# Optimization experiments

Measured on AMD Instinct MI355X. Metric: run time of the kernel, lower is better.

## Reference

```python
import jax, jax.numpy as jnp
import numpy as np

D_MODEL = 1024
NUM_HEADS = 16
HEAD_DIM = D_MODEL // NUM_HEADS
B, L = 4, 4096


def _linear(x, w, b):
    # torch nn.Linear: y = x @ w.T + b, w: [out, in]
    return jnp.einsum('bld,od->blo', x, w) + b


def _elu_feature_map(x):
    return jax.nn.elu(x) + 1.0


def setup_inputs() -> dict:
    key = jax.random.key(0)
    ks = jax.random.split(key, 11)
    s = 1.0 / np.sqrt(D_MODEL)
    inp = {
        'query': jax.random.normal(ks[0], (B, L, D_MODEL), jnp.float32),
        'key': jax.random.normal(ks[1], (B, L, D_MODEL), jnp.float32),
        'value': jax.random.normal(ks[2], (B, L, D_MODEL), jnp.float32),
        'wq': jax.random.uniform(ks[3], (D_MODEL, D_MODEL), jnp.float32, -s, s),
        'bq': jax.random.uniform(ks[4], (D_MODEL,), jnp.float32, -s, s),
        'wk': jax.random.uniform(ks[5], (D_MODEL, D_MODEL), jnp.float32, -s, s),
        'bk': jax.random.uniform(ks[6], (D_MODEL,), jnp.float32, -s, s),
        'wv': jax.random.uniform(ks[7], (D_MODEL, D_MODEL), jnp.float32, -s, s),
        'bv': jax.random.uniform(ks[8], (D_MODEL,), jnp.float32, -s, s),
        'wo': jax.random.uniform(ks[9], (D_MODEL, D_MODEL), jnp.float32, -s, s),
        'bo': jax.random.uniform(ks[10], (D_MODEL,), jnp.float32, -s, s),
    }
    return inp


def reference(query, key, value, wq, bq, wk, bk, wv, bv, wo, bo):
    Bsz, Lq, _ = query.shape
    # project and split heads -> [B, H, L, hd]
    def split_heads(x):
        return x.reshape(Bsz, -1, NUM_HEADS, HEAD_DIM).transpose(0, 2, 1, 3)
    Q = split_heads(_linear(query, wq, bq))
    K = split_heads(_linear(key, wk, bk))
    V = split_heads(_linear(value, wv, bv))
    Q = _elu_feature_map(Q)
    K = _elu_feature_map(K)
    # KV: [B, H, hd, hd]
    KV = jnp.einsum('bhld,bhle->bhde', K, V)
    Ksum = K.sum(axis=2)  # [B, H, hd]
    Z = 1.0 / (jnp.einsum('bhld,bhd->bhl', Q, Ksum) + 1e-6)  # [B, H, Lq]
    out = jnp.einsum('bhld,bhde->bhle', Q, KV) * Z[..., None]
    out = out.transpose(0, 2, 1, 3).reshape(Bsz, Lq, D_MODEL)
    return _linear(out, wo, bo)
```

## Files before the change

### kernel.cpp

```cpp
#include <hip/hip_runtime.h>
#include <hip/hip_bf16.h>

typedef _Float16 half8 __attribute__((ext_vector_type(8)));
typedef _Float16 half4 __attribute__((ext_vector_type(4)));
typedef float f32x4 __attribute__((ext_vector_type(4)));

#define KDIM 1024
#define NDIM 1024
#define MROWS 16384

#define GLD_LDS16(g, l)                                                  \
  __builtin_amdgcn_global_load_lds(                                      \
      (const __attribute__((address_space(1))) void*)(g),                \
      (__attribute__((address_space(3))) void*)(l), 16, 0, 0)

__global__ __launch_bounds__(256)
void cvt_f32_to_f16(const float* __restrict__ src, _Float16* __restrict__ dst,
                    int n8) {
  for (int i = blockIdx.x * 256 + threadIdx.x; i < n8; i += gridDim.x * 256) {
    float4 f0 = ((const float4*)src)[2 * i];
    float4 f1 = ((const float4*)src)[2 * i + 1];
    half8 h;
    h[0] = (_Float16)f0.x; h[1] = (_Float16)f0.y;
    h[2] = (_Float16)f0.z; h[3] = (_Float16)f0.w;
    h[4] = (_Float16)f1.x; h[5] = (_Float16)f1.y;
    h[6] = (_Float16)f1.z; h[7] = (_Float16)f1.w;
    ((half8*)dst)[i] = h;
  }
}

__global__ __launch_bounds__(256)
void cvt_w(const float* __restrict__ s0, _Float16* __restrict__ d0,
           const float* __restrict__ s1, _Float16* __restrict__ d1,
           const float* __restrict__ s2, _Float16* __restrict__ d2,
           const float* __restrict__ s3, _Float16* __restrict__ d3) {
  const float* src;
  _Float16* dst;
  switch (blockIdx.y) {
    case 0: src = s0; dst = d0; break;
    case 1: src = s1; dst = d1; break;
    case 2: src = s2; dst = d2; break;
    default: src = s3; dst = d3; break;
  }
  size_t i = (size_t)blockIdx.x * 256 + threadIdx.x;
  float4 f = ((const float4*)src)[i];
  half4 h;
  h[0] = (_Float16)f.x; h[1] = (_Float16)f.y;
  h[2] = (_Float16)f.z; h[3] = (_Float16)f.w;
  ((half4*)dst)[i] = h;
}

template <int ACT, int MODE, typename TOUT>
__global__ __launch_bounds__(512, 2)
void gemm_8ph(const _Float16* __restrict__ X, const _Float16* __restrict__ W,
              const float* __restrict__ bias, TOUT* __restrict__ Y,
              const _Float16* __restrict__ KVTx) {
  __shared__ char smem[131072];
  _Float16* As = (_Float16*)smem;
  _Float16* Bs = (_Float16*)(smem + 65536);

  const int tid  = threadIdx.x;
  const int lane = tid & 63;
  const int w    = tid >> 6;
  const int wm   = w >> 2;
  const int wn   = w & 3;

  const int bid = blockIdx.x;
  const int wid = (bid & 7) * 32 + (bid >> 3);
  const int m0  = (wid >> 2) * 256;
  const int n0  = (wid & 3) * 256;

  const int srow = lane >> 2;
  const int gsl  = (lane & 3) ^ ((lane >> 3) & 3);
  const _Float16* gA = X + (size_t)(m0 + w * 32 + srow) * KDIM + gsl * 8;
  const _Float16* gB = W + (size_t)(n0 + w * 32 + srow) * KDIM + gsl * 8;

#define STG(OPD, GSRC, T, KH, D)                                             \
  {                                                                          \
    _Float16* ldst = OPD + ((D) * 2 + (KH)) * 8192 + (w * 32) * 32;          \
    const _Float16* gs = GSRC + (size_t)(T) * 64 + (KH) * 32;                \
    GLD_LDS16(gs, ldst);                                                     \
    GLD_LDS16(gs + (size_t)16 * KDIM, ldst + 16 * 32);                       \
  }

  const int rsl = ((lane >> 4) ^ ((lane >> 1) & 3)) << 4;

#define RDA(DST, D, KH, MH)                                                  \
  _Pragma("unroll") for (int mi = 0; mi < 4; ++mi) {                         \
    int r = wm * 128 + (MH) * 64 + mi * 16 + (lane & 15);                    \
    DST[mi] = *(const half8*)((const char*)As + ((D) * 2 + (KH)) * 16384 +   \
                              r * 64 + rsl);                                 \
  }
#define RDB(D, KH)                                                           \
  _Pragma("unroll") for (int ni = 0; ni < 4; ++ni) {                         \
    int r = wn * 64 + ni * 16 + (lane & 15);                                 \
    b[ni] = *(const half8*)((const char*)Bs + ((D) * 2 + (KH)) * 16384 +     \
                            r * 64 + rsl);                                   \
  }
#define MM(AV, MH)                                                           \
  __builtin_amdgcn_s_setprio(1);                                             \
  _Pragma("unroll") for (int mi = 0; mi < 4; ++mi)                           \
    _Pragma("unroll") for (int ni = 0; ni < 4; ++ni)                         \
      acc[(MH) * 4 + mi][ni] = __builtin_amdgcn_mfma_f32_16x16x32_f16(       \
          AV[mi], b[ni], acc[(MH) * 4 + mi][ni], 0, 0, 0);                   \
  __builtin_amdgcn_s_setprio(0);

  f32x4 acc[8][4] = {};
  half8 a0[4], a1[4], b[4];

  STG(As, gA, 0, 0, 0); STG(Bs, gB, 0, 0, 0);
  STG(As, gA, 0, 1, 0); STG(Bs, gB, 0, 1, 0);

  for (int T = 0; T < 16; ++T) {
    const int d = T & 1, e = d ^ 1;
    asm volatile("s_waitcnt vmcnt(4)" ::: "memory");
    asm volatile("s_barrier" ::: "memory");
    RDA(a0, d, 0, 0);
    RDB(d, 0);
    if (T < 15) STG(As, gA, T + 1, 0, e);
    MM(a0, 0);
    RDA(a1, d, 0, 1);
    if (T < 15) STG(Bs, gB, T + 1, 0, e);
    MM(a1, 1);
    if (T < 15) { asm volatile("s_waitcnt vmcnt(4)" ::: "memory"); }
    else        { asm volatile("s_waitcnt vmcnt(0)" ::: "memory"); }
    asm volatile("s_barrier" ::: "memory");
    RDA(a0, d, 1, 0);
    RDB(d, 1);
    if (T < 15) STG(As, gA, T + 1, 1, e);
    MM(a0, 0);
    RDA(a1, d, 1, 1);
    if (T < 15) STG(Bs, gB, T + 1, 1, e);
    MM(a1, 1);
  }
#undef STG
#undef RDA
#undef RDB
#undef MM

  if constexpr (MODE == 2) {
    __syncthreads();
    _Float16* Cw = (_Float16*)(smem + w * 16384);
#pragma unroll
    for (int ni = 0; ni < 4; ++ni) {
      int dcol = ni * 16 + (lane & 15);
      float bv = bias[n0 + wn * 64 + dcol];
#pragma unroll
      for (int mi = 0; mi < 8; ++mi) {
#pragma unroll
        for (int i = 0; i < 4; ++i) {
          int rowr = mi * 16 + ((lane >> 4) << 2) + i;
          float v = acc[mi][ni][i] + bv;
          v = (v > 0.f) ? (v + 1.f) : __expf(v);
          int byte = rowr * 128 + dcol * 2;
          byte ^= (rowr & 7) << 4;
          *(_Float16*)((char*)Cw + byte) = (_Float16)v;
        }
      }
    }
    asm volatile("s_waitcnt lgkmcnt(0)" ::: "memory");
    __builtin_amdgcn_sched_barrier(0);
    const int bh0 = ((m0 >> 12) << 4) + (n0 >> 6);
    const _Float16* kvp = KVTx + (size_t)(bh0 + wn) * 5120;
#pragma unroll
    for (int half = 0; half < 2; ++half) {
      f32x4 acc2[4][5] = {};
#pragma unroll
      for (int kk = 0; kk < 2; ++kk) {
        half8 afr2[4], bfr2[5];
#pragma unroll
        for (int m = 0; m < 4; ++m) {
          int rowr = half * 64 + m * 16 + (lane & 15);
          int byte = rowr * 128 + kk * 64 + ((lane >> 4) << 4);
          byte ^= (rowr & 7) << 4;
          afr2[m] = *(const half8*)((const char*)Cw + byte);
        }
#pragma unroll
        for (int n = 0; n < 5; ++n) {
          int row = n * 16 + (lane & 15);
          bfr2[n] = *(const half8*)(kvp + row * 64 + kk * 32 + ((lane >> 4) << 3));
        }
#pragma unroll
        for (int m = 0; m < 4; ++m)
#pragma unroll
          for (int n = 0; n < 5; ++n)
            acc2[m][n] = __builtin_amdgcn_mfma_f32_16x16x32_f16(
                afr2[m], bfr2[n], acc2[m][n], 0, 0, 0);
      }
#pragma unroll
      for (int m = 0; m < 4; ++m) {
#pragma unroll
        for (int i = 0; i < 4; ++i) {
          float dn = __shfl(acc2[m][4][i], lane & 48);
          float z  = 1.f / (dn + 1e-6f);
          size_t row = (size_t)m0 + wm * 128 + half * 64 + m * 16 +
                       ((lane >> 4) << 2) + i;
#pragma unroll
          for (int n = 0; n < 4; ++n) {
            int col = n0 + wn * 64 + n * 16 + (lane & 15);
            Y[row * NDIM + col] = (TOUT)(acc2[m][n][i] * z);
          }
        }
      }
    }
    return;
  }

#pragma unroll
  for (int ni = 0; ni < 4; ++ni) {
    int col  = n0 + wn * 64 + ni * 16 + (lane & 15);
    float bv = bias[col];
#pragma unroll
    for (int mi = 0; mi < 8; ++mi) {
      int r0 = m0 + wm * 128 + mi * 16 + ((lane >> 4) << 2);
      if constexpr (MODE == 1) {
        int bb = r0 >> 12;
        int l0 = r0 & 4095;
        half4 hv;
#pragma unroll
        for (int i = 0; i < 4; ++i) {
          float v = acc[mi][ni][i] + bv;
          if constexpr (ACT == 1) v = (v > 0.f) ? (v + 1.f) : __expf(v);
          hv[i] = (_Float16)v;
        }
        *(half4*)((_Float16*)Y + ((size_t)(bb * 1024 + col)) * 4096 + l0) = hv;
      } else {
#pragma unroll
        for (int i = 0; i < 4; ++i) {
          float v = acc[mi][ni][i] + bv;
          if constexpr (ACT == 1) v = (v > 0.f) ? (v + 1.f) : __expf(v);
          Y[(size_t)(r0 + i) * NDIM + col] = (TOUT)v;
        }
      }
    }
  }
}

__global__ __launch_bounds__(256, 2)
void kv_mfma(const _Float16* __restrict__ KT, const _Float16* __restrict__ VT,
             _Float16* __restrict__ pKV) {
  const int bh = blockIdx.x;
  const int ch = blockIdx.y;
  const int tid  = threadIdx.x;
  const int lane = tid & 63;
  const int w    = tid >> 6;

  __shared__ _Float16 As[64 * 64];
  __shared__ _Float16 Bs[64 * 64];

  const int lr = lane >> 3;
  const int ls = (lane & 7) ^ lr;
  const size_t lbase = (size_t)ch * 1024 + ls * 8;
  const _Float16* gA = VT + (size_t)(bh * 64 + w * 16 + lr) * 4096 + lbase;
  const _Float16* gB = KT + (size_t)(bh * 64 + w * 16 + lr) * 4096 + lbase;
  _Float16* ldsA = As + (w * 16) * 64;
  _Float16* ldsB = Bs + (w * 16) * 64;

  half8 aones;
#pragma unroll
  for (int j = 0; j < 8; ++j) aones[j] = (lane & 15) == 0 ? (_Float16)1.0f : (_Float16)0.0f;

  f32x4 acc[5] = {};

  for (int k0 = 0; k0 < 1024; k0 += 64) {
    __syncthreads();
#pragma unroll
    for (int c = 0; c < 2; ++c) {
      GLD_LDS16(gA + k0 + (size_t)(c * 8) * 4096, ldsA + c * 8 * 64);
      GLD_LDS16(gB + k0 + (size_t)(c * 8) * 4096, ldsB + c * 8 * 64);
    }
    __syncthreads();

    half8 afr[4][2], bfr[2];
#pragma unroll
    for (int m = 0; m < 4; ++m)
#pragma unroll
      for (int kk = 0; kk < 2; ++kk) {
        int row  = m * 16 + (lane & 15);
        int byte = row * 128 + ((lane >> 4) << 4) + kk * 64;
        byte ^= (row & 7) << 4;
        afr[m][kk] = *(const half8*)((const char*)As + byte);
      }
#pragma unroll
    for (int kk = 0; kk < 2; ++kk) {
      int row  = w * 16 + (lane & 15);
      int byte = row * 128 + ((lane >> 4) << 4) + kk * 64;
      byte ^= (row & 7) << 4;
      bfr[kk] = *(const half8*)((const char*)Bs + byte);
    }
#pragma unroll
    for (int kk = 0; kk < 2; ++kk) {
#pragma unroll
      for (int m = 0; m < 4; ++m)
        acc[m] = __builtin_amdgcn_mfma_f32_16x16x32_f16(afr[m][kk], bfr[kk],
                                                        acc[m], 0, 0, 0);
      acc[4] = __builtin_amdgcn_mfma_f32_16x16x32_f16(aones, bfr[kk],
                                                      acc[4], 0, 0, 0);
    }
  }

  _Float16* outp = pKV + ((size_t)ch * 64 + bh) * 5120;
  const int col = w * 16 + (lane & 15);
#pragma unroll
  for (int m = 0; m < 5; ++m) {
#pragma unroll
    for (int i = 0; i < 4; ++i) {
      int row = m * 16 + ((lane >> 4) << 2) + i;
      outp[row * 64 + col] = (_Float16)acc[m][i];
    }
  }
}

__global__ __launch_bounds__(256)
void kv_combine(const _Float16* __restrict__ pKV, _Float16* __restrict__ KVTx) {
  int g = blockIdx.x * 256 + threadIdx.x;
  int bh = g / 5120;
  int j  = g - bh * 5120;
  float s = 0.f;
#pragma unroll
  for (int ch = 0; ch < 4; ++ch)
    s += (float)pKV[((size_t)ch * 64 + bh) * 5120 + j];
  KVTx[(size_t)bh * 5120 + j] = (_Float16)s;
}

extern "C" void kernel_launch(void* const* d_in, const int* in_sizes, int n_in,
                              void* d_out, int out_size, void* d_ws, size_t ws_size,
                              hipStream_t stream) {
  const float* q  = (const float*)d_in[0];
  const float* k  = (const float*)d_in[1];
  const float* v  = (const float*)d_in[2];
  const float* wq = (const float*)d_in[3];
  const float* bq = (const float*)d_in[4];
  const float* wk = (const float*)d_in[5];
  const float* bk = (const float*)d_in[6];
  const float* wv = (const float*)d_in[7];
  const float* bv = (const float*)d_in[8];
  const float* wo = (const float*)d_in[9];
  const float* bo = (const float*)d_in[10];
  float* out = (float*)d_out;

  char* ws = (char*)d_ws;
  _Float16* Xh   = (_Float16*)(ws);
  _Float16* KT   = (_Float16*)(ws + 33554432);
  _Float16* VT   = (_Float16*)(ws + 67108864);
  _Float16* pKV  = (_Float16*)(ws + 100663296);
  _Float16* whk  = (_Float16*)(ws + 100663296);
  _Float16* whv  = (_Float16*)(ws + 102760448);
  _Float16* whq  = (_Float16*)(ws + 104857600);
  _Float16* who  = (_Float16*)(ws + 106954752);
  _Float16* KVTx = (_Float16*)(ws + 109051904);
  _Float16* att  = KT;

  const int N8_BIG = MROWS * KDIM / 8;
  const int GBLK8  = (MROWS / 256) * (NDIM / 256);

  cvt_w<<<dim3(1024, 4), 256, 0, stream>>>(wq, whq, wk, whk, wv, whv, wo, who);

  cvt_f32_to_f16<<<4096, 256, 0, stream>>>(k, Xh, N8_BIG);
  gemm_8ph<1, 1, _Float16><<<GBLK8, 512, 0, stream>>>(Xh, whk, bk, KT, nullptr);
  cvt_f32_to_f16<<<4096, 256, 0, stream>>>(v, Xh, N8_BIG);
  gemm_8ph<0, 1, _Float16><<<GBLK8, 512, 0, stream>>>(Xh, whv, bv, VT, nullptr);

  kv_mfma<<<dim3(64, 4), 256, 0, stream>>>(KT, VT, pKV);
  kv_combine<<<1280, 256, 0, stream>>>(pKV, KVTx);

  cvt_f32_to_f16<<<4096, 256, 0, stream>>>(q, Xh, N8_BIG);
  gemm_8ph<1, 2, _Float16><<<GBLK8, 512, 0, stream>>>(Xh, whq, bq, att, KVTx);

  gemm_8ph<0, 0, float><<<GBLK8, 512, 0, stream>>>(att, who, bo, out, nullptr);
}
```

Before: 242.2 us.

## Fuse next input fp32-to-fp16 conversion into tail of preceding projection GEMM

The standalone conversion kernels for value and query are removed. Each projection GEMM now converts the next input tensor to fp16 after its epilogue, and the converted buffers are staged in the output buffer so they do not overwrite the current GEMM's input. This removes two kernel launches and lets the memory-bound conversion share the GEMM's launch, at the cost of running conversion work on the GEMM's heavy 512-thread blocks. It also relies on the output buffer being free until the final GEMM writes it.

```diff
diff --git a/kernel.cpp b/kernel.cpp
--- a/kernel.cpp
+++ b/kernel.cpp
@@ -50,11 +50,12 @@
   ((half4*)dst)[i] = h;
 }
 
-template <int ACT, int MODE, typename TOUT>
+template <int ACT, int MODE, int CVT, typename TOUT>
 __global__ __launch_bounds__(512, 2)
 void gemm_8ph(const _Float16* __restrict__ X, const _Float16* __restrict__ W,
               const float* __restrict__ bias, TOUT* __restrict__ Y,
-              const _Float16* __restrict__ KVTx) {
+              const _Float16* __restrict__ KVTx,
+              const float* __restrict__ csrc, _Float16* __restrict__ cdst) {
   __shared__ char smem[131072];
   _Float16* As = (_Float16*)smem;
   _Float16* Bs = (_Float16*)(smem + 65536);
@@ -234,6 +235,20 @@
       }
     }
   }
+
+  if constexpr (CVT) {
+    const int n8 = MROWS * KDIM / 8;
+    for (int i = bid * 512 + tid; i < n8; i += 256 * 512) {
+      float4 f0 = ((const float4*)csrc)[2 * i];
+      float4 f1 = ((const float4*)csrc)[2 * i + 1];
+      half8 h;
+      h[0] = (_Float16)f0.x; h[1] = (_Float16)f0.y;
+      h[2] = (_Float16)f0.z; h[3] = (_Float16)f0.w;
+      h[4] = (_Float16)f1.x; h[5] = (_Float16)f1.y;
+      h[6] = (_Float16)f1.z; h[7] = (_Float16)f1.w;
+      ((half8*)cdst)[i] = h;
+    }
+  }
 }
 
 __global__ __launch_bounds__(256, 2)
@@ -340,7 +355,7 @@
   float* out = (float*)d_out;
 
   char* ws = (char*)d_ws;
-  _Float16* Xh   = (_Float16*)(ws);
+  _Float16* Xk   = (_Float16*)(ws);
   _Float16* KT   = (_Float16*)(ws + 33554432);
   _Float16* VT   = (_Float16*)(ws + 67108864);
   _Float16* pKV  = (_Float16*)(ws + 100663296);
@@ -350,22 +365,27 @@
   _Float16* who  = (_Float16*)(ws + 106954752);
   _Float16* KVTx = (_Float16*)(ws + 109051904);
   _Float16* att  = KT;
+  _Float16* Xv   = (_Float16*)d_out;
+  _Float16* Xq   = (_Float16*)((char*)d_out + 33554432);
 
   const int N8_BIG = MROWS * KDIM / 8;
   const int GBLK8  = (MROWS / 256) * (NDIM / 256);
 
   cvt_w<<<dim3(1024, 4), 256, 0, stream>>>(wq, whq, wk, whk, wv, whv, wo, who);
 
-  cvt_f32_to_f16<<<4096, 256, 0, stream>>>(k, Xh, N8_BIG);
-  gemm_8ph<1, 1, _Float16><<<GBLK8, 512, 0, stream>>>(Xh, whk, bk, KT, nullptr);
-  cvt_f32_to_f16<<<4096, 256, 0, stream>>>(v, Xh, N8_BIG);
-  gemm_8ph<0, 1, _Float16><<<GBLK8, 512, 0, stream>>>(Xh, whv, bv, VT, nullptr);
+  cvt_f32_to_f16<<<4096, 256, 0, stream>>>(k, Xk, N8_BIG);
+
+  gemm_8ph<1, 1, 1, _Float16><<<GBLK8, 512, 0, stream>>>(
+      Xk, whk, bk, KT, nullptr, v, Xv);
+  gemm_8ph<0, 1, 1, _Float16><<<GBLK8, 512, 0, stream>>>(
+      Xv, whv, bv, VT, nullptr, q, Xq);
 
   kv_mfma<<<dim3(64, 4), 256, 0, stream>>>(KT, VT, pKV);
   kv_combine<<<1280, 256, 0, stream>>>(pKV, KVTx);
 
-  cvt_f32_to_f16<<<4096, 256, 0, stream>>>(q, Xh, N8_BIG);
-  gemm_8ph<1, 2, _Float16><<<GBLK8, 512, 0, stream>>>(Xh, whq, bq, att, KVTx);
-
-  gemm_8ph<0, 0, float><<<GBLK8, 512, 0, stream>>>(att, who, bo, out, nullptr);
-}
+  gemm_8ph<1, 2, 0, _Float16><<<GBLK8, 512, 0, stream>>>(
+      Xq, whq, bq, att, KVTx, nullptr, nullptr);
+
+  gemm_8ph<0, 0, 0, float><<<GBLK8, 512, 0, stream>>>(
+      att, who, bo, out, nullptr, nullptr, nullptr);
+}
```

Measured after the change: 237.8 us, median of 2. No clear change (-1.8%).
